# Kernel tuning notes

Measured on AMD Instinct MI355X. Metric: run time of the kernel, lower is better.

Reference implementation:

```python
import jax, jax.numpy as jnp
import numpy as np
from jax import lax

B, C, H, W = 32, 128, 56, 56
SIZE = C * H * W
EPS = 1e-5
SLOPE = 0.1


def setup_inputs() -> dict:
    key = jax.random.key(0)
    ks = jax.random.split(key, 12)
    return {
        "ax": jax.random.normal(ks[0], (B, C, H, W), dtype=jnp.float32),
        "mx": jax.random.normal(ks[1], (B, C, H, W), dtype=jnp.float32),
        # grouped conv1d (groups=SIZE, k=2, no bias) == per-position pair weights [SIZE, 2]
        "cfc_w": jax.random.normal(ks[2], (SIZE, 2), dtype=jnp.float32) * 0.1,
        # BatchNorm1d (eval mode) params over SIZE channels
        "bn_gamma": jax.random.normal(ks[3], (SIZE,), dtype=jnp.float32) * 0.1 + 1.0,
        "bn_beta": jax.random.normal(ks[4], (SIZE,), dtype=jnp.float32) * 0.1,
        "bn_mean": jax.random.normal(ks[5], (SIZE,), dtype=jnp.float32) * 0.1,
        "bn_var": jax.random.uniform(ks[6], (SIZE,), dtype=jnp.float32, minval=0.5, maxval=1.5),
        # conv3x3, C->C, bias
        "conv_w": jax.random.normal(ks[7], (C, C, 3, 3), dtype=jnp.float32) * (1.0 / np.sqrt(C * 9)),
        "conv_b": jax.random.normal(ks[8], (C,), dtype=jnp.float32) * 0.01,
        # BatchNorm2d (eval mode) params over C channels
        "bn2_gamma": jax.random.normal(ks[9], (C,), dtype=jnp.float32) * 0.1 + 1.0,
        "bn2_beta": jax.random.normal(ks[10], (C,), dtype=jnp.float32) * 0.1,
        "bn2_mean": jax.random.normal(ks[11], (C,), dtype=jnp.float32) * 0.1,
        "bn2_var": jax.random.uniform(jax.random.fold_in(key, 99), (C,), dtype=jnp.float32, minval=0.5, maxval=1.5),
    }


def reference(ax, mx, cfc_w, bn_gamma, bn_beta, bn_mean, bn_var,
              conv_w, conv_b, bn2_gamma, bn2_beta, bn2_mean, bn2_var):
    b, c, h, w = ax.shape
    a = ax.reshape(b, -1)  # [B, SIZE]
    m = mx.reshape(b, -1)
    # degenerate grouped Conv1d(k=2, groups=SIZE): z_i = w_i0 * a_i + w_i1 * m_i
    z = cfc_w[:, 0] * a + cfc_w[:, 1] * m
    # BatchNorm1d (eval) + LeakyReLU(0.1)
    z = (z - bn_mean) * (bn_gamma / jnp.sqrt(bn_var + EPS)) + bn_beta
    z = jax.nn.leaky_relu(z, SLOPE).reshape(b, c, h, w)
    # conv3x3 (stride 1, pad 1) + bias
    y = lax.conv_general_dilated(z, conv_w, window_strides=(1, 1),
                                 padding=((1, 1), (1, 1)),
                                 dimension_numbers=("NCHW", "OIHW", "NCHW"))
    y = y + conv_b[None, :, None, None]
    # BatchNorm2d (eval) + LeakyReLU(0.1)
    scale = (bn2_gamma / jnp.sqrt(bn2_var + EPS))[None, :, None, None]
    y = (y - bn2_mean[None, :, None, None]) * scale + bn2_beta[None, :, None, None]
    return jax.nn.leaky_relu(y, SLOPE)
```

## Files before the change

### kernel.cpp

```cpp
#include <hip/hip_runtime.h>

#define B_ 32
#define C_ 128
#define H_ 56
#define W_ 56
#define HW_ (H_*W_)
#define SIZE_ (C_*HW_)
#define NPIX_ (B_*HW_)
#define HP_ 58
#define WP_ 58
#define PLANE_ (HP_*WP_*C_)
#define K_ 1152
#define EPS_ 1e-5f
#define SLOPE_ 0.1f

typedef __bf16 bf16x8 __attribute__((ext_vector_type(8)));
typedef float  f32x4  __attribute__((ext_vector_type(4)));

__device__ __forceinline__ ushort f2bf(float x) {
    union { float f; unsigned u; } v; v.f = x;
    return (ushort)((v.u + 0x7FFFu + ((v.u >> 16) & 1u)) >> 16);
}
__device__ __forceinline__ float lrelu(float z) { return z > 0.f ? z : SLOPE_ * z; }

__device__ __forceinline__ void glds16(const ushort* g, ushort* l) {
    __builtin_amdgcn_global_load_lds(
        (const __attribute__((address_space(1))) unsigned int*)g,
        (__attribute__((address_space(3))) unsigned int*)l, 16, 0, 0);
}

__global__ __launch_bounds__(256) void prep_kernel(
    const float* __restrict__ conv_w, const float* __restrict__ conv_b,
    const float* __restrict__ g2, const float* __restrict__ b2,
    const float* __restrict__ m2, const float* __restrict__ v2,
    const float2* __restrict__ cfc, const float* __restrict__ g1,
    const float* __restrict__ b1, const float* __restrict__ mu1,
    const float* __restrict__ v1,
    ushort* __restrict__ wA, float* __restrict__ scale2, float* __restrict__ shift2,
    float* __restrict__ p0, float* __restrict__ p1, float* __restrict__ p2)
{
    int tid = blockIdx.x * 256 + threadIdx.x;
    if (tid < C_ * K_) {
        int co = tid / K_;
        int k  = tid - co * K_;
        int khkw = k >> 7, ci = k & 127;
        int kh = khkw / 3, kw = khkw - 3 * kh;
        wA[tid] = f2bf(conv_w[((co * C_ + ci) * 3 + kh) * 3 + kw]);
    }
    if (tid < C_) {
        float sc = g2[tid] * rsqrtf(v2[tid] + EPS_);
        scale2[tid] = sc;
        shift2[tid] = (conv_b[tid] - m2[tid]) * sc + b2[tid];
    }
    if (tid < SIZE_) {
        float sc = g1[tid] * rsqrtf(v1[tid] + EPS_);
        float2 wv = cfc[tid];
        p0[tid] = wv.x * sc;
        p1[tid] = wv.y * sc;
        p2[tid] = b1[tid] - mu1[tid] * sc;
    }
}

__global__ __launch_bounds__(256) void zfuse_kernel(
    const float4* __restrict__ ax, const float4* __restrict__ mx,
    const float4* __restrict__ p0, const float4* __restrict__ p1,
    const float4* __restrict__ p2, ushort* __restrict__ zp)
{
    __shared__ ushort tile[W_ * 132];
    const int hp = blockIdx.x, b = blockIdx.y;
    const int tid = threadIdx.x;
    ushort* row = zp + (size_t)b * PLANE_ + (size_t)hp * (WP_ * C_);
    if (hp == 0 || hp == HP_ - 1) {
        uint2* r2 = (uint2*)row;
        for (int i = tid; i < WP_ * C_ / 4; i += 256) r2[i] = make_uint2(0u, 0u);
        return;
    }
    const int h = hp - 1;
    const int base4 = (b * SIZE_) >> 2;
    for (int i = tid; i < 1792; i += 256) {
        int c  = i / 14;
        int w4 = i - c * 14;
        int s4 = c * (HW_ / 4) + h * (W_ / 4) + w4;
        float4 a = ax[base4 + s4];
        float4 m = mx[base4 + s4];
        float4 q0 = p0[s4], q1 = p1[s4], q2 = p2[s4];
        int wb = w4 * 4;
        tile[(wb + 0) * 132 + c] = f2bf(lrelu(a.x * q0.x + m.x * q1.x + q2.x));
        tile[(wb + 1) * 132 + c] = f2bf(lrelu(a.y * q0.y + m.y * q1.y + q2.y));
        tile[(wb + 2) * 132 + c] = f2bf(lrelu(a.z * q0.z + m.z * q1.z + q2.z));
        tile[(wb + 3) * 132 + c] = f2bf(lrelu(a.w * q0.w + m.w * q1.w + q2.w));
    }
    __syncthreads();
    if (tid < C_) {
        row[tid] = 0;
        row[(WP_ - 1) * C_ + tid] = 0;
    }
    for (int j = tid; j < 1792; j += 256) {
        int w = j >> 5, cc = j & 31;
        *(uint2*)(row + C_ + w * C_ + cc * 4) = *(const uint2*)(tile + w * 132 + cc * 4);
    }
}

__global__ __launch_bounds__(256) void conv_kernel(
    const ushort* __restrict__ zp, const ushort* __restrict__ wA,
    const float* __restrict__ scale2, const float* __restrict__ shift2,
    float* __restrict__ out)
{
    __shared__ ushort As[128 * 32];
    __shared__ ushort Bs[128 * 32];

    const int tid  = threadIdx.x;
    const int wave = tid >> 6, lane = tid & 63;
    const int l16  = lane & 15, quad = lane >> 4;
    const int pbase = blockIdx.x * 128;

    const int srow = wave * 32 + (lane >> 2);
    const int sch  = lane & 3;
    const ushort* agA = wA + srow * K_ + sch * 8;

    int pf0 = pbase + srow;
    int bb0 = pf0 / HW_, pi0 = pf0 - bb0 * HW_;
    int h0 = pi0 / W_, w0 = pi0 - h0 * W_;
    const ushort* bgB0 = zp + (size_t)bb0 * PLANE_ + (h0 * WP_ + w0) * C_ + sch * 8;
    int pf1 = pf0 + 16;
    int bb1 = pf1 / HW_, pi1 = pf1 - bb1 * HW_;
    int h1 = pi1 / W_, w1 = pi1 - h1 * W_;
    const ushort* bgB1 = zp + (size_t)bb1 * PLANE_ + (h1 * WP_ + w1) * C_ + sch * 8;

    ushort* lA0 = As + (wave * 32) * 32;
    ushort* lA1 = As + (wave * 32 + 16) * 32;
    ushort* lB0 = Bs + (wave * 32) * 32;
    ushort* lB1 = Bs + (wave * 32 + 16) * 32;

    const int cob = (wave & 1) * 64;
    const int pxb = (wave >> 1) * 64;

    f32x4 acc[4][4] = {};

    for (int tap = 0; tap < 9; ++tap) {
        const int kh = tap / 3, kw = tap - kh * 3;
        const int zoff = (kh * WP_ + kw) * C_;
        const int aoff = tap * C_;
        #pragma unroll
        for (int ks = 0; ks < 4; ++ks) {
            const int ko = ks * 32;
            __syncthreads();
            glds16(agA + aoff + ko,            lA0);
            glds16(agA + 16 * K_ + aoff + ko,  lA1);
            glds16(bgB0 + zoff + ko,           lB0);
            glds16(bgB1 + zoff + ko,           lB1);
            __syncthreads();
            bf16x8 af[4], bfr[4];
            #pragma unroll
            for (int mt = 0; mt < 4; ++mt)
                af[mt] = *(const bf16x8*)(As + (cob + mt * 16 + l16) * 32 + quad * 8);
            #pragma unroll
            for (int nt = 0; nt < 4; ++nt)
                bfr[nt] = *(const bf16x8*)(Bs + (pxb + nt * 16 + l16) * 32 + quad * 8);
            #pragma unroll
            for (int mt = 0; mt < 4; ++mt)
                #pragma unroll
                for (int nt = 0; nt < 4; ++nt)
                    acc[mt][nt] = __builtin_amdgcn_mfma_f32_16x16x32_bf16(
                        af[mt], bfr[nt], acc[mt][nt], 0, 0, 0);
        }
    }

    int pob[4];
    #pragma unroll
    for (int nt = 0; nt < 4; ++nt) {
        int pf = pbase + pxb + nt * 16 + l16;
        int bb = pf / HW_;
        pob[nt] = bb * SIZE_ + (pf - bb * HW_);
    }
    #pragma unroll
    for (int mt = 0; mt < 4; ++mt) {
        #pragma unroll
        for (int r = 0; r < 4; ++r) {
            int co = cob + mt * 16 + quad * 4 + r;
            float sc = scale2[co], sh = shift2[co];
            #pragma unroll
            for (int nt = 0; nt < 4; ++nt) {
                float v = acc[mt][nt][r] * sc + sh;
                out[(size_t)pob[nt] + co * HW_] = lrelu(v);
            }
        }
    }
}

extern "C" void kernel_launch(void* const* d_in, const int* in_sizes, int n_in,
                              void* d_out, int out_size, void* d_ws, size_t ws_size,
                              hipStream_t stream) {
    const float* ax     = (const float*)d_in[0];
    const float* mx     = (const float*)d_in[1];
    const float* cfc    = (const float*)d_in[2];
    const float* bn_g   = (const float*)d_in[3];
    const float* bn_b   = (const float*)d_in[4];
    const float* bn_m   = (const float*)d_in[5];
    const float* bn_v   = (const float*)d_in[6];
    const float* conv_w = (const float*)d_in[7];
    const float* conv_b = (const float*)d_in[8];
    const float* g2     = (const float*)d_in[9];
    const float* b2     = (const float*)d_in[10];
    const float* m2     = (const float*)d_in[11];
    const float* v2     = (const float*)d_in[12];
    float* out = (float*)d_out;

    char* ws = (char*)d_ws;
    ushort* zp     = (ushort*)ws;
    ushort* wA     = (ushort*)(ws + 27557888);
    float*  scale2 = (float*)(ws + 27852800);
    float*  shift2 = (float*)(ws + 27853312);
    float*  p0     = (float*)(ws + 27853824);
    float*  p1     = (float*)(ws + 29459456);
    float*  p2     = (float*)(ws + 31065088);

    prep_kernel<<<dim3((SIZE_ + 255) / 256), 256, 0, stream>>>(
        conv_w, conv_b, g2, b2, m2, v2, (const float2*)cfc,
        bn_g, bn_b, bn_m, bn_v, wA, scale2, shift2, p0, p1, p2);
    zfuse_kernel<<<dim3(HP_, B_), 256, 0, stream>>>(
        (const float4*)ax, (const float4*)mx,
        (const float4*)p0, (const float4*)p1, (const float4*)p2, zp);
    conv_kernel<<<dim3(NPIX_ / 128), 256, 0, stream>>>(zp, wA, scale2, shift2, out);
}
```

Measured before the change: 236.5 us.

## Double-buffer conv LDS stages, swizzle LDS layout, remap blocks, repack zfuse tile

The conv kernel now uses two LDS buffers, so the global-to-LDS load for the next K-slice is issued before the MFMAs on the current slice, with one barrier per step instead of two. It also XOR-swizzles the 16-byte chunk index in LDS to reduce bank conflicts on fragment reads, and remaps block indices into an interleaved order. The zfuse kernel stores its tile channel-major with packed 32-bit writes and transposes on the read side. The costs are twice the LDS use, which may lower occupancy, and possible bank conflicts on the new strided zfuse reads.

```diff
diff --git a/kernel.cpp b/kernel.cpp
--- a/kernel.cpp
+++ b/kernel.cpp
@@ -66,7 +66,7 @@
     const float4* __restrict__ p0, const float4* __restrict__ p1,
     const float4* __restrict__ p2, ushort* __restrict__ zp)
 {
-    __shared__ ushort tile[W_ * 132];
+    __shared__ ushort tile[C_ * 58];
     const int hp = blockIdx.x, b = blockIdx.y;
     const int tid = threadIdx.x;
     ushort* row = zp + (size_t)b * PLANE_ + (size_t)hp * (WP_ * C_);
@@ -84,20 +84,25 @@
         float4 a = ax[base4 + s4];
         float4 m = mx[base4 + s4];
         float4 q0 = p0[s4], q1 = p1[s4], q2 = p2[s4];
-        int wb = w4 * 4;
-        tile[(wb + 0) * 132 + c] = f2bf(lrelu(a.x * q0.x + m.x * q1.x + q2.x));
-        tile[(wb + 1) * 132 + c] = f2bf(lrelu(a.y * q0.y + m.y * q1.y + q2.y));
-        tile[(wb + 2) * 132 + c] = f2bf(lrelu(a.z * q0.z + m.z * q1.z + q2.z));
-        tile[(wb + 3) * 132 + c] = f2bf(lrelu(a.w * q0.w + m.w * q1.w + q2.w));
+        uint z0 = f2bf(lrelu(a.x * q0.x + m.x * q1.x + q2.x));
+        uint z1 = f2bf(lrelu(a.y * q0.y + m.y * q1.y + q2.y));
+        uint z2 = f2bf(lrelu(a.z * q0.z + m.z * q1.z + q2.z));
+        uint z3 = f2bf(lrelu(a.w * q0.w + m.w * q1.w + q2.w));
+        uint* t32 = (uint*)(tile + c * 58 + w4 * 4);
+        t32[0] = z0 | (z1 << 16);
+        t32[1] = z2 | (z3 << 16);
     }
     __syncthreads();
-    if (tid < C_) {
-        row[tid] = 0;
-        row[(WP_ - 1) * C_ + tid] = 0;
+    if (tid < 64) {
+        int side = tid >> 5, cc = tid & 31;
+        *(uint2*)(row + side * (57 * C_) + cc * 4) = make_uint2(0u, 0u);
     }
     for (int j = tid; j < 1792; j += 256) {
-        int w = j >> 5, cc = j & 31;
-        *(uint2*)(row + C_ + w * C_ + cc * 4) = *(const uint2*)(tile + w * 132 + cc * 4);
+        int w  = j >> 5;
+        int c0 = (j & 31) * 4;
+        uint lo = (uint)tile[(c0 + 0) * 58 + w] | ((uint)tile[(c0 + 1) * 58 + w] << 16);
+        uint hi = (uint)tile[(c0 + 2) * 58 + w] | ((uint)tile[(c0 + 3) * 58 + w] << 16);
+        *(uint2*)(row + (w + 1) * C_ + c0) = make_uint2(lo, hi);
     }
 }
 
@@ -106,17 +111,18 @@
     const float* __restrict__ scale2, const float* __restrict__ shift2,
     float* __restrict__ out)
 {
-    __shared__ ushort As[128 * 32];
-    __shared__ ushort Bs[128 * 32];
+    __shared__ ushort As[2 * 4096];
+    __shared__ ushort Bs[2 * 4096];
 
     const int tid  = threadIdx.x;
     const int wave = tid >> 6, lane = tid & 63;
     const int l16  = lane & 15, quad = lane >> 4;
-    const int pbase = blockIdx.x * 128;
+    const int blk  = blockIdx.x;
+    const int pbase = ((blk & 7) * 98 + (blk >> 3)) * 128;
 
     const int srow = wave * 32 + (lane >> 2);
-    const int sch  = lane & 3;
-    const ushort* agA = wA + srow * K_ + sch * 8;
+    const int sch  = (lane & 3) ^ ((lane >> 3) & 3);
+    const ushort* agA0 = wA + srow * K_ + sch * 8;
 
     int pf0 = pbase + srow;
     int bb0 = pf0 / HW_, pi0 = pf0 - bb0 * HW_;
@@ -127,43 +133,47 @@
     int h1 = pi1 / W_, w1 = pi1 - h1 * W_;
     const ushort* bgB1 = zp + (size_t)bb1 * PLANE_ + (h1 * WP_ + w1) * C_ + sch * 8;
 
-    ushort* lA0 = As + (wave * 32) * 32;
-    ushort* lA1 = As + (wave * 32 + 16) * 32;
-    ushort* lB0 = Bs + (wave * 32) * 32;
-    ushort* lB1 = Bs + (wave * 32 + 16) * 32;
+    ushort* aD = As + wave * 1024;
+    ushort* bD = Bs + wave * 1024;
+
+    auto stage = [&](int s, int buf) {
+        int tap = s >> 2;
+        int ko  = (s & 3) * 32;
+        int kh  = tap / 3, kw = tap - 3 * kh;
+        int aoff = tap * C_ + ko;
+        int boff = (kh * WP_ + kw) * C_ + ko;
+        glds16(agA0 + aoff,           aD + buf * 4096);
+        glds16(agA0 + 16 * K_ + aoff, aD + buf * 4096 + 512);
+        glds16(bgB0 + boff,           bD + buf * 4096);
+        glds16(bgB1 + boff,           bD + buf * 4096 + 512);
+    };
 
     const int cob = (wave & 1) * 64;
     const int pxb = (wave >> 1) * 64;
+    const int swq = (quad ^ ((l16 >> 1) & 3)) * 8;
 
     f32x4 acc[4][4] = {};
-
-    for (int tap = 0; tap < 9; ++tap) {
-        const int kh = tap / 3, kw = tap - kh * 3;
-        const int zoff = (kh * WP_ + kw) * C_;
-        const int aoff = tap * C_;
-        #pragma unroll
-        for (int ks = 0; ks < 4; ++ks) {
-            const int ko = ks * 32;
-            __syncthreads();
-            glds16(agA + aoff + ko,            lA0);
-            glds16(agA + 16 * K_ + aoff + ko,  lA1);
-            glds16(bgB0 + zoff + ko,           lB0);
-            glds16(bgB1 + zoff + ko,           lB1);
-            __syncthreads();
-            bf16x8 af[4], bfr[4];
-            #pragma unroll
-            for (int mt = 0; mt < 4; ++mt)
-                af[mt] = *(const bf16x8*)(As + (cob + mt * 16 + l16) * 32 + quad * 8);
+    stage(0, 0);
+    #pragma unroll 2
+    for (int s = 0; s < 36; ++s) {
+        const int cur = s & 1;
+        __syncthreads();
+        if (s < 35) stage(s + 1, cur ^ 1);
+        const ushort* Ab = As + cur * 4096;
+        const ushort* Bb = Bs + cur * 4096;
+        bf16x8 af[4], bfr[4];
+        #pragma unroll
+        for (int mt = 0; mt < 4; ++mt)
+            af[mt] = *(const bf16x8*)(Ab + (cob + mt * 16 + l16) * 32 + swq);
+        #pragma unroll
+        for (int nt = 0; nt < 4; ++nt)
+            bfr[nt] = *(const bf16x8*)(Bb + (pxb + nt * 16 + l16) * 32 + swq);
+        #pragma unroll
+        for (int mt = 0; mt < 4; ++mt)
             #pragma unroll
             for (int nt = 0; nt < 4; ++nt)
-                bfr[nt] = *(const bf16x8*)(Bs + (pxb + nt * 16 + l16) * 32 + quad * 8);
-            #pragma unroll
-            for (int mt = 0; mt < 4; ++mt)
-                #pragma unroll
-                for (int nt = 0; nt < 4; ++nt)
-                    acc[mt][nt] = __builtin_amdgcn_mfma_f32_16x16x32_bf16(
-                        af[mt], bfr[nt], acc[mt][nt], 0, 0, 0);
-        }
+                acc[mt][nt] = __builtin_amdgcn_mfma_f32_16x16x32_bf16(
+                    af[mt], bfr[nt], acc[mt][nt], 0, 0, 0);
     }
 
     int pob[4];
```

New measurement: 237.9 us. No clear change (+0.6%).
